# Kernel tuning notes

Measured on AMD Instinct MI355X. Metric: run time of the kernel, lower is better.

Reference implementation:

```python
import jax, jax.numpy as jnp
import numpy as np

N_NODES = 100000
N_EDGES = 800000
IN_DIM, HID_DIM, OUT_DIM = 128, 256, 128


def setup_inputs() -> dict:
    key = jax.random.key(0)
    ks = jax.random.split(key, 8)
    x = jax.random.normal(ks[0], (N_NODES, IN_DIM), dtype=jnp.float32)
    edge_index = jax.random.randint(ks[1], (2, N_EDGES), 0, N_NODES, dtype=jnp.int32)
    s = lambda k, shp, fan_in: jax.random.normal(k, shp, dtype=jnp.float32) / np.sqrt(fan_in)
    return {
        "x": x,
        "edge_index": edge_index,
        "W1_l": s(ks[2], (HID_DIM, IN_DIM), IN_DIM),   # applied to aggregated neighbors
        "b1": jnp.zeros((HID_DIM,), jnp.float32),
        "W1_r": s(ks[3], (HID_DIM, IN_DIM), IN_DIM),   # root/self transform (no bias, as in PyG)
        "W2_l": s(ks[4], (OUT_DIM, HID_DIM), HID_DIM),
        "b2": jnp.zeros((OUT_DIM,), jnp.float32),
        "W2_r": s(ks[5], (OUT_DIM, HID_DIM), HID_DIM),
    }


def _sage_conv(x, src, dst, W_l, b, W_r):
    # mean aggregation of source-neighbor features onto targets
    msg = x[src]                                              # [E, d]
    agg = jax.ops.segment_sum(msg, dst, num_segments=N_NODES)  # [N, d]
    cnt = jax.ops.segment_sum(jnp.ones((src.shape[0],), x.dtype), dst, num_segments=N_NODES)
    mean = agg / jnp.maximum(cnt, 1.0)[:, None]
    # SAGEConv: lin_l(aggr) + lin_r(x)
    return mean @ W_l.T + b + x @ W_r.T


def reference(x, edge_index, W1_l, b1, W1_r, W2_l, b2, W2_r):
    src, dst = edge_index[0], edge_index[1]
    h = jax.nn.relu(_sage_conv(x, src, dst, W1_l, b1, W1_r))
    # dropout p=0.0 -> identity (eval-mode equivalent)
    out = _sage_conv(h, src, dst, W2_l, b2, W2_r)
    return out
```

## Files before the change

kernel.cpp:

```cpp
#include <hip/hip_runtime.h>

#define NN 100000
#define NE 800000

typedef __attribute__((ext_vector_type(4))) float f32x4;
typedef __attribute__((ext_vector_type(4))) int   i32x4;
typedef __attribute__((ext_vector_type(8))) unsigned short u16x8;

__device__ __forceinline__ unsigned short f2bf(float f) {
  unsigned u = __float_as_uint(f);
  return (unsigned short)((u + 0x7FFFu + ((u >> 16) & 1u)) >> 16);
}
__device__ __forceinline__ float bf2f(unsigned short b) {
  return __uint_as_float(((unsigned)b) << 16);
}

__global__ void degree_k(const int* __restrict__ dst, int* __restrict__ deg,
                         int* __restrict__ rord) {
  int e = blockIdx.x * 256 + threadIdx.x;
  if (e < NE) {
    int o = atomicAdd(&deg[dst[e]], 1);
    __builtin_nontemporal_store(o, &rord[e]);
  }
}

__global__ __launch_bounds__(256) void scan1_k(const int* __restrict__ deg,
    int* __restrict__ offs, int* __restrict__ bsum, float* __restrict__ inv) {
  __shared__ int s[256];
  int t = threadIdx.x;
  int base = blockIdx.x * 1024 + t * 4;
  int v[4], tsum = 0;
#pragma unroll
  for (int k = 0; k < 4; ++k) {
    int i = base + k;
    v[k] = (i < NN) ? deg[i] : 0;
    tsum += v[k];
    if (i < NN) inv[i] = 1.0f / fmaxf((float)v[k], 1.0f);
  }
  s[t] = tsum; __syncthreads();
  int val = tsum;
#pragma unroll
  for (int off = 1; off < 256; off <<= 1) {
    int x = (t >= off) ? s[t - off] : 0;
    __syncthreads();
    val += x; s[t] = val;
    __syncthreads();
  }
  int excl = val - tsum;
  if (t == 255) bsum[blockIdx.x] = val;
  int run = excl;
#pragma unroll
  for (int k = 0; k < 4; ++k) { int i = base + k; if (i < NN) offs[i] = run; run += v[k]; }
}

__global__ __launch_bounds__(256) void scan2_k(int* __restrict__ bsum, int nb) {
  __shared__ int s[256];
  int t = threadIdx.x;
  int v = (t < nb) ? bsum[t] : 0;
  s[t] = v; __syncthreads();
  int val = v;
#pragma unroll
  for (int off = 1; off < 256; off <<= 1) {
    int x = (t >= off) ? s[t - off] : 0;
    __syncthreads();
    val += x; s[t] = val;
    __syncthreads();
  }
  if (t < nb) bsum[t] = val - v;
}

__global__ __launch_bounds__(256) void scan3_k(int* __restrict__ offs,
    const int* __restrict__ bsum) {
  int base = blockIdx.x * 1024 + threadIdx.x * 4;
  int add = bsum[blockIdx.x];
#pragma unroll
  for (int k = 0; k < 4; ++k) {
    int i = base + k;
    if (i < NN) offs[i] += add;
  }
}

__global__ void fill_k(const int* __restrict__ src, const int* __restrict__ dst,
    const int* __restrict__ offs, const int* __restrict__ rord,
    int* __restrict__ eidx) {
  int e = blockIdx.x * 256 + threadIdx.x;
  if (e < NE) {
    int p = offs[dst[e]] + rord[e];
    __builtin_nontemporal_store(src[e], &eidx[p]);
  }
}

#define NXV (NN * 128 / 4)
__global__ __launch_bounds__(256) void cast_all_k(const float* __restrict__ x,
    const float* __restrict__ Wa, const float* __restrict__ Wbm,
    const float* __restrict__ Wc, const float* __restrict__ Wd,
    unsigned short* __restrict__ xb, unsigned short* __restrict__ Wbo) {
  int i = blockIdx.x * 256 + threadIdx.x;
  if (i < NXV) {
    float4 v = *reinterpret_cast<const float4*>(x + (size_t)i * 4);
    ushort4 o;
    o.x = f2bf(v.x); o.y = f2bf(v.y); o.z = f2bf(v.z); o.w = f2bf(v.w);
    *reinterpret_cast<ushort4*>(xb + (size_t)i * 4) = o;
  } else {
    int k = i - NXV;
    if (k < 4 * 32768) {
      int seg = k >> 15, off = k & 32767;
      const float* s = (seg < 2) ? (seg == 0 ? Wa : Wbm) : (seg == 2 ? Wc : Wd);
      Wbo[k] = f2bf(s[off]);
    }
  }
}

template<int GMODE>
__global__ __launch_bounds__(256) void gather_k(const unsigned short* __restrict__ feat,
    const int* __restrict__ offs, const int* __restrict__ deg,
    const float* __restrict__ inv, const int* __restrict__ eidx,
    const unsigned short* __restrict__ selfb,
    unsigned short* __restrict__ outb, float* __restrict__ outf) {
  int node = blockIdx.x * 16 + (threadIdx.x >> 4);
  int l = threadIdx.x & 15;
  if (node >= NN) return;
  int st = offs[node], n = deg[node];
  float a[8];
#pragma unroll
  for (int k = 0; k < 8; ++k) a[k] = 0.f;

  int j = 0;
  for (; j + 8 <= n; j += 8) {
    int si[8];
#pragma unroll
    for (int q = 0; q < 8; ++q) si[q] = eidx[st + j + q];
    u16x8 r[8];
#pragma unroll
    for (int q = 0; q < 8; ++q)
      r[q] = *reinterpret_cast<const u16x8*>(feat + (size_t)si[q] * 128 + l * 8);
#pragma unroll
    for (int q = 0; q < 8; ++q)
#pragma unroll
      for (int k = 0; k < 8; ++k) a[k] += bf2f(r[q][k]);
  }
  for (; j + 4 <= n; j += 4) {
    int si[4];
#pragma unroll
    for (int q = 0; q < 4; ++q) si[q] = eidx[st + j + q];
    u16x8 r[4];
#pragma unroll
    for (int q = 0; q < 4; ++q)
      r[q] = *reinterpret_cast<const u16x8*>(feat + (size_t)si[q] * 128 + l * 8);
#pragma unroll
    for (int q = 0; q < 4; ++q)
#pragma unroll
      for (int k = 0; k < 8; ++k) a[k] += bf2f(r[q][k]);
  }
  for (; j < n; ++j) {
    int s = eidx[st + j];
    u16x8 r = *reinterpret_cast<const u16x8*>(feat + (size_t)s * 128 + l * 8);
#pragma unroll
    for (int k = 0; k < 8; ++k) a[k] += bf2f(r[k]);
  }

  float sc = inv[node];
  if (GMODE == 2) {
    u16x8 sb = *reinterpret_cast<const u16x8*>(selfb + (size_t)node * 128 + l * 8);
    float4 o0, o1;
    o0.x = bf2f(sb[0]) + sc * a[0]; o0.y = bf2f(sb[1]) + sc * a[1];
    o0.z = bf2f(sb[2]) + sc * a[2]; o0.w = bf2f(sb[3]) + sc * a[3];
    o1.x = bf2f(sb[4]) + sc * a[4]; o1.y = bf2f(sb[5]) + sc * a[5];
    o1.z = bf2f(sb[6]) + sc * a[6]; o1.w = bf2f(sb[7]) + sc * a[7];
    float* po = outf + (size_t)node * 128 + l * 8;
    *reinterpret_cast<float4*>(po) = o0;
    *reinterpret_cast<float4*>(po + 4) = o1;
  } else {
    u16x8 o;
#pragma unroll
    for (int k = 0; k < 8; ++k) o[k] = f2bf(sc * a[k]);
    *reinterpret_cast<u16x8*>(outb + (size_t)node * 128 + l * 8) = o;
  }
}

template<int MODE>
__global__ __launch_bounds__(256, 2) void mgemm_k(
    const unsigned short* __restrict__ A1, const unsigned short* __restrict__ A2,
    const unsigned short* __restrict__ Wbase, const float* __restrict__ bias,
    unsigned short* __restrict__ outb, unsigned short* __restrict__ outb2) {
  __shared__ unsigned short As[2][64 * 256];
  const int t = threadIdx.x;
  const int wave = t >> 6, lane = t & 63;
  const int lhi = lane >> 4, llo = lane & 15;

  i32x4 bfrag[8][4];
  float bv[4];
#pragma unroll
  for (int fn = 0; fn < 4; ++fn) {
    int c = wave * 64 + fn * 16 + llo;
    const unsigned short* rowp;
    if (MODE == 0) {
      rowp = Wbase + (size_t)c * 128;
      bv[fn] = bias[c];
    } else {
      rowp = Wbase + (wave >= 2 ? 32768 : 0) + (size_t)(c & 127) * 256;
      bv[fn] = (wave >= 2) ? bias[c & 127] : 0.f;
    }
#pragma unroll
    for (int ks = 0; ks < 8; ++ks) {
      int koff = (MODE == 0) ? ((ks & 3) * 32 + lhi * 8 + ((ks >= 4) ? 32768 : 0))
                             : (ks * 32 + lhi * 8);
      bfrag[ks][fn] = *reinterpret_cast<const i32x4*>(rowp + koff);
    }
  }

  auto stage = [&](int buf, int row0) {
#pragma unroll
    for (int c = 0; c < 8; ++c) {
      int chunk = wave * 8 + c;
      int tb = chunk * 1024 + lane * 16;
      int r = tb >> 9;
      int cb = tb & 511;
      int cbs = cb ^ ((r & 7) << 4);
      int gr = min(row0 + r, NN - 1);
      const char* gsrc;
      if (MODE == 0) {
        const unsigned short* Asel = (cbs < 256) ? A1 : A2;
        gsrc = (const char*)(Asel + (size_t)gr * 128) + (cbs & 255);
      } else {
        gsrc = (const char*)(A1 + (size_t)gr * 256) + cbs;
      }
      __builtin_amdgcn_global_load_lds(
          (const __attribute__((address_space(1))) void*)gsrc,
          (__attribute__((address_space(3))) void*)((char*)As + buf * 32768 + chunk * 1024),
          16, 0, 0);
    }
  };

  const int npan = (NN + 63) >> 6;
  int p = blockIdx.x;
  stage(0, p * 64);
  int cur = 0;

#pragma unroll 1
  for (; p < npan; p += gridDim.x) {
    int pn = p + gridDim.x;
    if (pn < npan) stage(cur ^ 1, pn * 64);
    asm volatile("s_waitcnt vmcnt(8)" ::: "memory");
    __builtin_amdgcn_s_barrier();

    const int row0 = p * 64;
    f32x4 acc[4][4];
#pragma unroll
    for (int fm = 0; fm < 4; ++fm)
#pragma unroll
      for (int fn = 0; fn < 4; ++fn) acc[fm][fn] = (f32x4)0.f;

#pragma unroll
    for (int ks = 0; ks < 8; ++ks) {
      i32x4 a[4];
#pragma unroll
      for (int fm = 0; fm < 4; ++fm) {
        int r = fm * 16 + llo;
        int cb = (ks * 64 + lhi * 16) ^ ((r & 7) << 4);
        a[fm] = *reinterpret_cast<const i32x4*>((const char*)As + cur * 32768 + r * 512 + cb);
      }
#pragma unroll
      for (int fm = 0; fm < 4; ++fm)
#pragma unroll
        for (int fn = 0; fn < 4; ++fn)
          asm("v_mfma_f32_16x16x32_bf16 %0, %1, %2, %0"
              : "+v"(acc[fm][fn]) : "v"(a[fm]), "v"(bfrag[ks][fn]));
    }

    asm volatile("s_nop 7\n\ts_nop 7");

#pragma unroll
    for (int fm = 0; fm < 4; ++fm) {
#pragma unroll
      for (int fn = 0; fn < 4; ++fn) {
        int col = wave * 64 + fn * 16 + llo;
#pragma unroll
        for (int j = 0; j < 4; ++j) {
          int row = row0 + fm * 16 + lhi * 4 + j;
          if (row < NN) {
            float v = acc[fm][fn][j] + bv[fn];
            if (MODE == 0) {
              v = fmaxf(v, 0.f);
              outb[(size_t)row * 256 + col] = f2bf(v);
            } else if (wave < 2) {
              outb[(size_t)row * 128 + col] = f2bf(v);
            } else {
              outb2[(size_t)row * 128 + (col - 128)] = f2bf(v);
            }
          }
        }
      }
    }
    __builtin_amdgcn_s_barrier();
    cur ^= 1;
  }
}

extern "C" void kernel_launch(void* const* d_in, const int* in_sizes, int n_in,
                              void* d_out, int out_size, void* d_ws, size_t ws_size,
                              hipStream_t stream) {
  const float* x   = (const float*)d_in[0];
  const int*   ei  = (const int*)d_in[1];
  const float* W1l = (const float*)d_in[2];
  const float* b1  = (const float*)d_in[3];
  const float* W1r = (const float*)d_in[4];
  const float* W2l = (const float*)d_in[5];
  const float* b2  = (const float*)d_in[6];
  const float* W2r = (const float*)d_in[7];
  float* out = (float*)d_out;

  char* ws = (char*)d_ws;
  float*          inv    = (float*)(ws);
  int*            deg    = (int*)(ws + 0x80000);
  int*            offs   = (int*)(ws + 0x100000);
  int*            bsum   = (int*)(ws + 0x200000);
  unsigned short* Wb     = (unsigned short*)(ws + 0x280000);
  int*            eidx   = (int*)(ws + 0x400000);
  unsigned short* xb     = (unsigned short*)(ws + 0x800000);
  unsigned short* m1b    = (unsigned short*)(ws + 0x2200000);
  unsigned short* hb     = (unsigned short*)(ws + 0x3C00000);
  unsigned short* hWb    = (unsigned short*)(ws + 0x6E00000);
  int*            rord   = (int*)(ws + 0x8600000);
  unsigned short* selfb  = m1b;

  const int* src = ei;
  const int* dst = ei + NE;
  const int NB = (NN + 1023) / 1024;

  hipMemsetAsync(deg, 0, NN * sizeof(int), stream);
  degree_k<<<(NE + 255) / 256, 256, 0, stream>>>(dst, deg, rord);
  scan1_k<<<NB, 256, 0, stream>>>(deg, offs, bsum, inv);
  scan2_k<<<1, 256, 0, stream>>>(bsum, NB);
  scan3_k<<<NB, 256, 0, stream>>>(offs, bsum);
  fill_k<<<(NE + 255) / 256, 256, 0, stream>>>(src, dst, offs, rord, eidx);

  cast_all_k<<<(NXV + 4 * 32768 + 255) / 256, 256, 0, stream>>>(x, W1l, W1r, W2l, W2r, xb, Wb);

  gather_k<0><<<(NN + 15) / 16, 256, 0, stream>>>(xb, offs, deg, inv, eidx, nullptr, m1b, nullptr);
  mgemm_k<0><<<512, 256, 0, stream>>>(m1b, xb, Wb, b1, hb, nullptr);

  mgemm_k<1><<<512, 256, 0, stream>>>(hb, nullptr, Wb + 65536, b2, hWb, selfb);
  gather_k<2><<<(NN + 15) / 16, 256, 0, stream>>>(hWb, offs, deg, inv, eidx, selfb, nullptr, out);
}
```

Measured before the change: 228.8 us.

## Fuse preprocessing kernels and use grid-stride gathers with nontemporal output stores

```diff
diff --git a/kernel.cpp b/kernel.cpp
--- a/kernel.cpp
+++ b/kernel.cpp
@@ -15,12 +15,33 @@
   return __uint_as_float(((unsigned)b) << 16);
 }
 
-__global__ void degree_k(const int* __restrict__ dst, int* __restrict__ deg,
-                         int* __restrict__ rord) {
-  int e = blockIdx.x * 256 + threadIdx.x;
-  if (e < NE) {
+#define NBDEG 3125
+#define NXV   (NN * 128 / 4)
+#define NBX   12500
+#define NBW   512
+__global__ __launch_bounds__(256) void prep_k(
+    const float* __restrict__ x,
+    const float* __restrict__ Wa, const float* __restrict__ Wbm,
+    const float* __restrict__ Wc, const float* __restrict__ Wd,
+    const int* __restrict__ dst,
+    unsigned short* __restrict__ xb, unsigned short* __restrict__ Wbo,
+    int* __restrict__ deg, int* __restrict__ rord) {
+  int bid = blockIdx.x, t = threadIdx.x;
+  if (bid < NBDEG) {
+    int e = bid * 256 + t;
     int o = atomicAdd(&deg[dst[e]], 1);
     __builtin_nontemporal_store(o, &rord[e]);
+  } else if (bid < NBDEG + NBX) {
+    int i = (bid - NBDEG) * 256 + t;
+    float4 v = *reinterpret_cast<const float4*>(x + (size_t)i * 4);
+    ushort4 o;
+    o.x = f2bf(v.x); o.y = f2bf(v.y); o.z = f2bf(v.z); o.w = f2bf(v.w);
+    *reinterpret_cast<ushort4*>(xb + (size_t)i * 4) = o;
+  } else {
+    int k = (bid - NBDEG - NBX) * 256 + t;
+    int seg = k >> 15, off = k & 32767;
+    const float* s = (seg < 2) ? (seg == 0 ? Wa : Wbm) : (seg == 2 ? Wc : Wd);
+    Wbo[k] = f2bf(s[off]);
   }
 }
 
@@ -69,44 +90,27 @@
   if (t < nb) bsum[t] = val - v;
 }
 
-__global__ __launch_bounds__(256) void scan3_k(int* __restrict__ offs,
-    const int* __restrict__ bsum) {
-  int base = blockIdx.x * 1024 + threadIdx.x * 4;
-  int add = bsum[blockIdx.x];
-#pragma unroll
-  for (int k = 0; k < 4; ++k) {
-    int i = base + k;
-    if (i < NN) offs[i] += add;
-  }
-}
-
-__global__ void fill_k(const int* __restrict__ src, const int* __restrict__ dst,
-    const int* __restrict__ offs, const int* __restrict__ rord,
-    int* __restrict__ eidx) {
-  int e = blockIdx.x * 256 + threadIdx.x;
-  if (e < NE) {
-    int p = offs[dst[e]] + rord[e];
-    __builtin_nontemporal_store(src[e], &eidx[p]);
-  }
-}
-
-#define NXV (NN * 128 / 4)
-__global__ __launch_bounds__(256) void cast_all_k(const float* __restrict__ x,
-    const float* __restrict__ Wa, const float* __restrict__ Wbm,
-    const float* __restrict__ Wc, const float* __restrict__ Wd,
-    unsigned short* __restrict__ xb, unsigned short* __restrict__ Wbo) {
-  int i = blockIdx.x * 256 + threadIdx.x;
-  if (i < NXV) {
-    float4 v = *reinterpret_cast<const float4*>(x + (size_t)i * 4);
-    ushort4 o;
-    o.x = f2bf(v.x); o.y = f2bf(v.y); o.z = f2bf(v.z); o.w = f2bf(v.w);
-    *reinterpret_cast<ushort4*>(xb + (size_t)i * 4) = o;
+#define NBFIN 98
+__global__ __launch_bounds__(256) void finfill_k(
+    const int* __restrict__ offs, const int* __restrict__ bsum,
+    int* __restrict__ offs2,
+    const int* __restrict__ src, const int* __restrict__ dst,
+    const int* __restrict__ rord, int* __restrict__ eidx) {
+  int bid = blockIdx.x, t = threadIdx.x;
+  if (bid < NBFIN) {
+    int base = bid * 1024 + t * 4;
+    int add = bsum[bid];
+#pragma unroll
+    for (int k = 0; k < 4; ++k) {
+      int i = base + k;
+      if (i < NN) offs2[i] = offs[i] + add;
+    }
   } else {
-    int k = i - NXV;
-    if (k < 4 * 32768) {
-      int seg = k >> 15, off = k & 32767;
-      const float* s = (seg < 2) ? (seg == 0 ? Wa : Wbm) : (seg == 2 ? Wc : Wd);
-      Wbo[k] = f2bf(s[off]);
+    int e = (bid - NBFIN) * 256 + t;
+    if (e < NE) {
+      int d = dst[e];
+      int p = offs[d] + bsum[d >> 10] + rord[e];
+      __builtin_nontemporal_store(src[e], &eidx[p]);
     }
   }
 }
@@ -117,64 +121,66 @@
     const float* __restrict__ inv, const int* __restrict__ eidx,
     const unsigned short* __restrict__ selfb,
     unsigned short* __restrict__ outb, float* __restrict__ outf) {
-  int node = blockIdx.x * 16 + (threadIdx.x >> 4);
-  int l = threadIdx.x & 15;
-  if (node >= NN) return;
-  int st = offs[node], n = deg[node];
-  float a[8];
-#pragma unroll
-  for (int k = 0; k < 8; ++k) a[k] = 0.f;
-
-  int j = 0;
-  for (; j + 8 <= n; j += 8) {
-    int si[8];
-#pragma unroll
-    for (int q = 0; q < 8; ++q) si[q] = eidx[st + j + q];
-    u16x8 r[8];
-#pragma unroll
-    for (int q = 0; q < 8; ++q)
-      r[q] = *reinterpret_cast<const u16x8*>(feat + (size_t)si[q] * 128 + l * 8);
-#pragma unroll
-    for (int q = 0; q < 8; ++q)
-#pragma unroll
-      for (int k = 0; k < 8; ++k) a[k] += bf2f(r[q][k]);
-  }
-  for (; j + 4 <= n; j += 4) {
-    int si[4];
-#pragma unroll
-    for (int q = 0; q < 4; ++q) si[q] = eidx[st + j + q];
-    u16x8 r[4];
-#pragma unroll
-    for (int q = 0; q < 4; ++q)
-      r[q] = *reinterpret_cast<const u16x8*>(feat + (size_t)si[q] * 128 + l * 8);
-#pragma unroll
-    for (int q = 0; q < 4; ++q)
-#pragma unroll
-      for (int k = 0; k < 8; ++k) a[k] += bf2f(r[q][k]);
-  }
-  for (; j < n; ++j) {
-    int s = eidx[st + j];
-    u16x8 r = *reinterpret_cast<const u16x8*>(feat + (size_t)s * 128 + l * 8);
-#pragma unroll
-    for (int k = 0; k < 8; ++k) a[k] += bf2f(r[k]);
-  }
-
-  float sc = inv[node];
-  if (GMODE == 2) {
-    u16x8 sb = *reinterpret_cast<const u16x8*>(selfb + (size_t)node * 128 + l * 8);
-    float4 o0, o1;
-    o0.x = bf2f(sb[0]) + sc * a[0]; o0.y = bf2f(sb[1]) + sc * a[1];
-    o0.z = bf2f(sb[2]) + sc * a[2]; o0.w = bf2f(sb[3]) + sc * a[3];
-    o1.x = bf2f(sb[4]) + sc * a[4]; o1.y = bf2f(sb[5]) + sc * a[5];
-    o1.z = bf2f(sb[6]) + sc * a[6]; o1.w = bf2f(sb[7]) + sc * a[7];
-    float* po = outf + (size_t)node * 128 + l * 8;
-    *reinterpret_cast<float4*>(po) = o0;
-    *reinterpret_cast<float4*>(po + 4) = o1;
-  } else {
-    u16x8 o;
-#pragma unroll
-    for (int k = 0; k < 8; ++k) o[k] = f2bf(sc * a[k]);
-    *reinterpret_cast<u16x8*>(outb + (size_t)node * 128 + l * 8) = o;
+  const int l = threadIdx.x & 15;
+  for (int nb = blockIdx.x * 16; nb < NN; nb += gridDim.x * 16) {
+    int node = nb + (threadIdx.x >> 4);
+    if (node >= NN) continue;
+    int st = offs[node], n = deg[node];
+    float a[8];
+#pragma unroll
+    for (int k = 0; k < 8; ++k) a[k] = 0.f;
+
+    int j = 0;
+    for (; j + 8 <= n; j += 8) {
+      int si[8];
+#pragma unroll
+      for (int q = 0; q < 8; ++q) si[q] = eidx[st + j + q];
+      u16x8 r[8];
+#pragma unroll
+      for (int q = 0; q < 8; ++q)
+        r[q] = *reinterpret_cast<const u16x8*>(feat + (size_t)si[q] * 128 + l * 8);
+#pragma unroll
+      for (int q = 0; q < 8; ++q)
+#pragma unroll
+        for (int k = 0; k < 8; ++k) a[k] += bf2f(r[q][k]);
+    }
+    for (; j + 4 <= n; j += 4) {
+      int si[4];
+#pragma unroll
+      for (int q = 0; q < 4; ++q) si[q] = eidx[st + j + q];
+      u16x8 r[4];
+#pragma unroll
+      for (int q = 0; q < 4; ++q)
+        r[q] = *reinterpret_cast<const u16x8*>(feat + (size_t)si[q] * 128 + l * 8);
+#pragma unroll
+      for (int q = 0; q < 4; ++q)
+#pragma unroll
+        for (int k = 0; k < 8; ++k) a[k] += bf2f(r[q][k]);
+    }
+    for (; j < n; ++j) {
+      int s = eidx[st + j];
+      u16x8 r = *reinterpret_cast<const u16x8*>(feat + (size_t)s * 128 + l * 8);
+#pragma unroll
+      for (int k = 0; k < 8; ++k) a[k] += bf2f(r[k]);
+    }
+
+    float sc = inv[node];
+    if (GMODE == 2) {
+      u16x8 sb = *reinterpret_cast<const u16x8*>(selfb + (size_t)node * 128 + l * 8);
+      f32x4 o0, o1;
+      o0[0] = bf2f(sb[0]) + sc * a[0]; o0[1] = bf2f(sb[1]) + sc * a[1];
+      o0[2] = bf2f(sb[2]) + sc * a[2]; o0[3] = bf2f(sb[3]) + sc * a[3];
+      o1[0] = bf2f(sb[4]) + sc * a[4]; o1[1] = bf2f(sb[5]) + sc * a[5];
+      o1[2] = bf2f(sb[6]) + sc * a[6]; o1[3] = bf2f(sb[7]) + sc * a[7];
+      float* po = outf + (size_t)node * 128 + l * 8;
+      __builtin_nontemporal_store(o0, reinterpret_cast<f32x4*>(po));
+      __builtin_nontemporal_store(o1, reinterpret_cast<f32x4*>(po + 4));
+    } else {
+      u16x8 o;
+#pragma unroll
+      for (int k = 0; k < 8; ++k) o[k] = f2bf(sc * a[k]);
+      *reinterpret_cast<u16x8*>(outb + (size_t)node * 128 + l * 8) = o;
+    }
   }
 }
 
@@ -314,6 +320,7 @@
   float*          inv    = (float*)(ws);
   int*            deg    = (int*)(ws + 0x80000);
   int*            offs   = (int*)(ws + 0x100000);
+  int*            offs2  = (int*)(ws + 0x180000);
   int*            bsum   = (int*)(ws + 0x200000);
   unsigned short* Wb     = (unsigned short*)(ws + 0x280000);
   int*            eidx   = (int*)(ws + 0x400000);
@@ -329,17 +336,16 @@
   const int NB = (NN + 1023) / 1024;
 
   hipMemsetAsync(deg, 0, NN * sizeof(int), stream);
-  degree_k<<<(NE + 255) / 256, 256, 0, stream>>>(dst, deg, rord);
+  prep_k<<<NBDEG + NBX + NBW, 256, 0, stream>>>(x, W1l, W1r, W2l, W2r, dst,
+                                                xb, Wb, deg, rord);
   scan1_k<<<NB, 256, 0, stream>>>(deg, offs, bsum, inv);
   scan2_k<<<1, 256, 0, stream>>>(bsum, NB);
-  scan3_k<<<NB, 256, 0, stream>>>(offs, bsum);
-  fill_k<<<(NE + 255) / 256, 256, 0, stream>>>(src, dst, offs, rord, eidx);
-
-  cast_all_k<<<(NXV + 4 * 32768 + 255) / 256, 256, 0, stream>>>(x, W1l, W1r, W2l, W2r, xb, Wb);
-
-  gather_k<0><<<(NN + 15) / 16, 256, 0, stream>>>(xb, offs, deg, inv, eidx, nullptr, m1b, nullptr);
+  finfill_k<<<NBFIN + (NE + 255) / 256, 256, 0, stream>>>(offs, bsum, offs2,
+                                                          src, dst, rord, eidx);
+
+  gather_k<0><<<2048, 256, 0, stream>>>(xb, offs2, deg, inv, eidx, nullptr, m1b, nullptr);
   mgemm_k<0><<<512, 256, 0, stream>>>(m1b, xb, Wb, b1, hb, nullptr);
 
   mgemm_k<1><<<512, 256, 0, stream>>>(hb, nullptr, Wb + 65536, b2, hWb, selfb);
-  gather_k<2><<<(NN + 15) / 16, 256, 0, stream>>>(hWb, offs, deg, inv, eidx, selfb, nullptr, out);
-}
+  gather_k<2><<<2048, 256, 0, stream>>>(hWb, offs2, deg, inv, eidx, selfb, nullptr, out);
+}
```

Result: no change. 224.9 us (-1.7%).
